# Optimization experiments

Measured on AMD Instinct MI355X. Metric: run time of the kernel, lower is better.

The kernel has to match this reference:

```python
import jax, jax.numpy as jnp
import numpy as np

B, S, H = 2, 2048, 2048
NH, NKV, D = 16, 4, 128      # heads, kv heads, head_dim
GROUPS = NH // NKV
WIN = 1024                    # sliding window
EPS = 1e-5
THETA = 10000.0
NEG = -1e9


def _rms_norm(x, w):
    # over last dim (head_dim)
    var = jnp.mean(x * x, axis=-1, keepdims=True)
    return x * jax.lax.rsqrt(var + EPS) * w


def _rotate_half(x):
    x1, x2 = jnp.split(x, 2, axis=-1)
    return jnp.concatenate([-x2, x1], axis=-1)


def _apply_rope(q, k, cos, sin):
    # q: [B,NH,S,D], k: [B,NKV,S,D], cos/sin: [B,S,D]
    c = cos[:, None, :, :]
    s = sin[:, None, :, :]
    q = q * c + _rotate_half(q) * s
    k = k * c + _rotate_half(k) * s
    return q, k


def setup_inputs() -> dict:
    key = jax.random.key(0)
    ks = jax.random.split(key, 8)
    std = 0.02
    hidden_states = jax.random.normal(ks[0], (B, S, H), dtype=jnp.float32)
    Wq = jax.random.normal(ks[1], (NH * D, H), dtype=jnp.float32) * std
    Wk = jax.random.normal(ks[2], (NKV * D, H), dtype=jnp.float32) * std
    Wv = jax.random.normal(ks[3], (NKV * D, H), dtype=jnp.float32) * std
    Wo = jax.random.normal(ks[4], (H, NH * D), dtype=jnp.float32) * std
    Wg = jax.random.normal(ks[5], (NH * D, H), dtype=jnp.float32) * std
    q_norm_w = jnp.ones((D,), dtype=jnp.float32)
    k_norm_w = jnp.ones((D,), dtype=jnp.float32)
    # RoPE tables
    inv_freq = 1.0 / (THETA ** (jnp.arange(0, D, 2, dtype=jnp.float32) / D))
    pos = jnp.arange(S, dtype=jnp.float32)
    freqs = jnp.einsum('s,d->sd', pos, inv_freq)          # [S, D/2]
    emb = jnp.concatenate([freqs, freqs], axis=-1)        # [S, D]
    cos = jnp.broadcast_to(jnp.cos(emb)[None], (B, S, D)).astype(jnp.float32)
    sin = jnp.broadcast_to(jnp.sin(emb)[None], (B, S, D)).astype(jnp.float32)
    i = jnp.arange(S)[:, None]
    j = jnp.arange(S)[None, :]
    allowed = (j <= i) & (i - j < WIN)
    attention_mask = jnp.where(allowed, 0.0, NEG).astype(jnp.float32)[None, None]  # [1,1,S,S]
    return {
        'hidden_states': hidden_states, 'cos': cos, 'sin': sin,
        'attention_mask': attention_mask,
        'Wq': Wq, 'Wk': Wk, 'Wv': Wv, 'Wo': Wo, 'Wg': Wg,
        'q_norm_w': q_norm_w, 'k_norm_w': k_norm_w,
    }


def reference(hidden_states, cos, sin, attention_mask, Wq, Wk, Wv, Wo, Wg, q_norm_w, k_norm_w):
    x = hidden_states                                  # [B,S,H]
    q = (x @ Wq.T).reshape(B, S, NH, D)
    k = (x @ Wk.T).reshape(B, S, NKV, D)
    v = (x @ Wv.T).reshape(B, S, NKV, D)
    gate = x @ Wg.T                                    # [B,S,NH*D]
    q = _rms_norm(q, q_norm_w)
    k = _rms_norm(k, k_norm_w)
    q = q.transpose(0, 2, 1, 3)                        # [B,NH,S,D]
    k = k.transpose(0, 2, 1, 3)                        # [B,NKV,S,D]
    v = v.transpose(0, 2, 1, 3)
    # local (sliding) attention layer -> RoPE applied
    q, k = _apply_rope(q, k, cos, sin)
    # GQA: repeat kv heads
    k = jnp.repeat(k, GROUPS, axis=1)                  # [B,NH,S,D]
    v = jnp.repeat(v, GROUPS, axis=1)
    scaling = D ** -0.5
    scores = jnp.einsum('bhqd,bhkd->bhqk', q, k) * scaling
    scores = scores + attention_mask                   # broadcast [1,1,S,S]
    probs = jax.nn.softmax(scores.astype(jnp.float32), axis=-1).astype(q.dtype)
    out = jnp.einsum('bhqk,bhkd->bhqd', probs, v)      # [B,NH,S,D]
    out = out.transpose(0, 2, 1, 3).reshape(B, S, NH * D)
    out = out * jax.nn.sigmoid(gate)
    return out @ Wo.T                                  # [B,S,H]
```

## Files before the change

### kernel.cpp

```cpp
#include <hip/hip_runtime.h>
#include <hip/hip_bf16.h>

#define B_    2
#define S_    2048
#define H_    2048
#define NH_   16
#define NKV_  4
#define D_    128
#define WIN_  1024

typedef __attribute__((ext_vector_type(8))) short short8;
typedef __attribute__((ext_vector_type(4))) float f32x4;

__device__ __forceinline__ void gl2lds16(const void* g, void* l) {
  __builtin_amdgcn_global_load_lds(
      (const __attribute__((address_space(1))) void*)g,
      (__attribute__((address_space(3))) void*)l, 16, 0, 0);
}

__device__ __forceinline__ unsigned short f2bf(float x) {
  union { float f; unsigned int u; } v; v.f = x;
  unsigned int r = v.u + 0x7fffu + ((v.u >> 16) & 1u);
  return (unsigned short)(r >> 16);
}
__device__ __forceinline__ float bf2f(unsigned short u) {
  union { unsigned int i; float f; } v; v.i = ((unsigned int)u) << 16; return v.f;
}

#define CVT_TOTAL 5767168L
__global__ __launch_bounds__(256) void convert_all(
    const float* __restrict__ hs, const float* __restrict__ wq,
    const float* __restrict__ wk, const float* __restrict__ wv,
    const float* __restrict__ wg, const float* __restrict__ wo,
    unsigned short* __restrict__ xb, unsigned short* __restrict__ wall,
    unsigned short* __restrict__ wob) {
  long i = (long)blockIdx.x * 256 + threadIdx.x;
  if (i >= CVT_TOTAL) return;
  const float4* src; ushort4* dst;
  if (i < 2097152)      { src = (const float4*)hs + i;                         dst = (ushort4*)xb + i; }
  else if (i < 3145728) { long j = i - 2097152; src = (const float4*)wq + j;   dst = (ushort4*)wall + j; }
  else if (i < 3407872) { long j = i - 3145728; src = (const float4*)wk + j;   dst = (ushort4*)wall + 1048576 + j; }
  else if (i < 3670016) { long j = i - 3407872; src = (const float4*)wv + j;   dst = (ushort4*)wall + 1310720 + j; }
  else if (i < 4718592) { long j = i - 3670016; src = (const float4*)wg + j;   dst = (ushort4*)wall + 1572864 + j; }
  else                  { long j = i - 4718592; src = (const float4*)wo + j;   dst = (ushort4*)wob + j; }
  float4 v = *src;
  ushort4 o; o.x = f2bf(v.x); o.y = f2bf(v.y); o.z = f2bf(v.z); o.w = f2bf(v.w);
  *dst = o;
}

template <bool OUT_BF16>
__global__ __launch_bounds__(256) void gemm_bt(
    const unsigned short* __restrict__ A,
    const unsigned short* __restrict__ Bm,
    void* __restrict__ Cv, int M, int N, int K)
{
  __shared__ unsigned short As[128 * 64];
  __shared__ unsigned short Bs[128 * 64];
  const int t = threadIdx.x;
  const int lane = t & 63, wave = t >> 6;
  const int quad = lane >> 4, rl = lane & 15;
  const int bm = blockIdx.x * 128, bn = blockIdx.y * 128;
  const int wm = (wave >> 1) * 64, wn = (wave & 1) * 64;
  const int ldsbase = (t & ~63) * 8;

  f32x4 acc[4][4];
#pragma unroll
  for (int i = 0; i < 4; i++)
#pragma unroll
    for (int j = 0; j < 4; j++) acc[i][j] = (f32x4){0.f, 0.f, 0.f, 0.f};

  for (int k0 = 0; k0 < K; k0 += 64) {
#pragma unroll
    for (int i = 0; i < 4; i++) {
      int tt = i * 256 + t;
      int row = tt >> 3;
      int lc = (tt & 7) ^ (row & 7);
      gl2lds16(A + (long)(bm + row) * K + k0 + lc * 8, As + i * 2048 + ldsbase);
      gl2lds16(Bm + (long)(bn + row) * K + k0 + lc * 8, Bs + i * 2048 + ldsbase);
    }
    __syncthreads();
#pragma unroll
    for (int kk = 0; kk < 2; kk++) {
      short8 af[4], bfr[4];
#pragma unroll
      for (int i = 0; i < 4; i++) {
        int row = wm + i * 16 + rl;
        af[i] = *(const short8*)(As + row * 64 + (((kk * 4 + quad) ^ (row & 7)) * 8));
      }
#pragma unroll
      for (int j = 0; j < 4; j++) {
        int row = wn + j * 16 + rl;
        bfr[j] = *(const short8*)(Bs + row * 64 + (((kk * 4 + quad) ^ (row & 7)) * 8));
      }
#pragma unroll
      for (int i = 0; i < 4; i++)
#pragma unroll
        for (int j = 0; j < 4; j++)
          acc[i][j] = __builtin_amdgcn_mfma_f32_16x16x32_bf16(af[i], bfr[j], acc[i][j], 0, 0, 0);
    }
    __syncthreads();
  }
#pragma unroll
  for (int i = 0; i < 4; i++) {
    int row0 = bm + wm + i * 16 + quad * 4;
#pragma unroll
    for (int j = 0; j < 4; j++) {
      int col = bn + wn + j * 16 + rl;
#pragma unroll
      for (int r = 0; r < 4; r++) {
        if (OUT_BF16)
          ((unsigned short*)Cv)[(long)(row0 + r) * N + col] = f2bf(acc[i][j][r]);
        else
          ((float*)Cv)[(long)(row0 + r) * N + col] = acc[i][j][r];
      }
    }
  }
}

__global__ __launch_bounds__(256) void pack_and_transpose(
    const unsigned short* __restrict__ qkvg,
    const float* __restrict__ cosb, const float* __restrict__ sinb,
    const float* __restrict__ qw, const float* __restrict__ kw,
    unsigned short* __restrict__ qb, unsigned short* __restrict__ kb,
    unsigned short* __restrict__ vt)
{
  __shared__ unsigned short tile[64][136];
  int t = threadIdx.x;
  if (blockIdx.x >= 20480) {
    int blk = blockIdx.x - 20480;
    int st = blk & 31, kv = (blk >> 5) & 3, b = blk >> 7;
    int s0 = st * 64;
#pragma unroll
    for (int i = 0; i < 4; i++) {
      int idx = i * 256 + t;
      int r = idx >> 4, c = (idx & 15) * 8;
      short8 v = *(const short8*)(qkvg + (long)(b * S_ + s0 + r) * 5120 + 2560 + kv * 128 + c);
      *(short8*)(&tile[r][c]) = v;
    }
    __syncthreads();
    long vo = (long)(b * NKV_ + kv) * 128;
#pragma unroll
    for (int i = 0; i < 8; i++) {
      int idx = i * 256 + t;
      int d = idx >> 4, sc = idx & 15;
      ushort4 o;
      o.x = tile[sc * 4 + 0][d]; o.y = tile[sc * 4 + 1][d];
      o.z = tile[sc * 4 + 2][d]; o.w = tile[sc * 4 + 3][d];
      *(ushort4*)(vt + (vo + d) * S_ + s0 + sc * 4) = o;
    }
    return;
  }
  int lane = t & 63, wave = t >> 6;
  long gw = (long)blockIdx.x * 4 + wave;
  int hu = (int)(gw % 20);
  long bs = gw / 20;
  int b = (int)(bs / S_);
  int s = (int)(bs % S_);
  const unsigned short* row = qkvg + bs * 5120;

  bool isq = hu < 16;
  const unsigned short* base = isq ? (row + hu * 128) : (row + 2048 + (hu - 16) * 128);
  float x1 = bf2f(base[lane]), x2 = bf2f(base[lane + 64]);
  float ss = x1 * x1 + x2 * x2;
#pragma unroll
  for (int m = 1; m < 64; m <<= 1) ss += __shfl_xor(ss, m, 64);
  float inv = rsqrtf(ss * (1.0f / 128.0f) + 1e-5f);
  const float* w = isq ? qw : kw;
  float n1 = x1 * inv * w[lane], n2 = x2 * inv * w[lane + 64];
  const float* cp = cosb + bs * 128;
  const float* sp = sinb + bs * 128;
  float o1 = n1 * cp[lane] - n2 * sp[lane];
  float o2 = n2 * cp[lane + 64] + n1 * sp[lane + 64];
  if (isq) {
    long o = ((long)(b * NH_ + hu) * S_ + s) * 128;
    qb[o + lane] = f2bf(o1); qb[o + lane + 64] = f2bf(o2);
  } else {
    long o = ((long)(b * NKV_ + (hu - 16)) * S_ + s) * 128;
    kb[o + lane] = f2bf(o1); kb[o + lane + 64] = f2bf(o2);
  }
}

#define KSTR 136
#define VSTR 72
#define PSTR 68
__global__ __launch_bounds__(256, 3) void attn_kernel(
    const unsigned short* __restrict__ qb,
    const unsigned short* __restrict__ kbuf,
    const unsigned short* __restrict__ vt,
    const unsigned short* __restrict__ qkvg,
    unsigned short* __restrict__ aout)
{
  __shared__ unsigned short Ks[64 * KSTR];
  __shared__ unsigned short Vs[128 * VSTR];
  __shared__ unsigned short Ps[4][16 * PSTR];
  int t = threadIdx.x, lane = t & 63, wave = t >> 6;
  int quad = lane >> 4, rl = lane & 15;
  int blk = blockIdx.x;
  int qt = 31 - (blk >> 5);
  int qu = blk & 3;
  int kv = (blk >> 2) & 3;
  int b  = (blk >> 4) & 1;
  int h = kv * 4 + wave;
  int q0 = qt * 64 + qu * 16;

  const unsigned short* qhead = qb + (((long)(b * NH_ + h)) * S_) * 128;
  short8 qf[4];
#pragma unroll
  for (int ks = 0; ks < 4; ks++)
    qf[ks] = *(const short8*)(qhead + (long)(q0 + rl) * 128 + ks * 32 + quad * 8);

  f32x4 oacc[8];
#pragma unroll
  for (int j = 0; j < 8; j++) oacc[j] = (f32x4){0.f, 0.f, 0.f, 0.f};
  float m_r[4], l_r[4];
#pragma unroll
  for (int r = 0; r < 4; r++) { m_r[r] = -1e9f; l_r[r] = 0.f; }

  const unsigned short* kbase_p = kbuf + ((long)(b * NKV_ + kv)) * S_ * 128;
  const unsigned short* vbase_p = vt + ((long)(b * NKV_ + kv)) * 128 * S_;
  int t_lo = qt - 16; if (t_lo < 0) t_lo = 0;

  int kr[4], kc[4], vr[4], vc[4];
#pragma unroll
  for (int i = 0; i < 4; i++) {
    int idx = i * 256 + t;
    kr[i] = idx >> 4; kc[i] = (idx & 15) * 8;
    vr[i] = idx >> 3; vc[i] = (idx & 7) * 8;
  }

  {
    int kb0 = t_lo * 64;
    short8 kv0[4], vv0[4];
#pragma unroll
    for (int i = 0; i < 4; i++) {
      kv0[i] = *(const short8*)(kbase_p + (long)(kb0 + kr[i]) * 128 + kc[i]);
      vv0[i] = *(const short8*)(vbase_p + (long)vr[i] * S_ + kb0 + vc[i]);
    }
#pragma unroll
    for (int i = 0; i < 4; i++) {
      *(short8*)(Ks + kr[i] * KSTR + kc[i]) = kv0[i];
      *(short8*)(Vs + vr[i] * VSTR + vc[i]) = vv0[i];
    }
  }
  __syncthreads();

  const float scale = 0.08838834764831845f;
  for (int kt = t_lo; kt <= qt; ++kt) {
    int kb0 = kt * 64;
    short8 kpre[4], vpre[4];
    if (kt < qt) {
      int nb0 = kb0 + 64;
#pragma unroll
      for (int i = 0; i < 4; i++) {
        kpre[i] = *(const short8*)(kbase_p + (long)(nb0 + kr[i]) * 128 + kc[i]);
        vpre[i] = *(const short8*)(vbase_p + (long)vr[i] * S_ + nb0 + vc[i]);
      }
    }

    f32x4 sc[4];
    __builtin_amdgcn_s_setprio(1);
#pragma unroll
    for (int nt = 0; nt < 4; nt++) {
      f32x4 c0 = (f32x4){0.f, 0.f, 0.f, 0.f};
#pragma unroll
      for (int ks = 0; ks < 4; ks++) {
        short8 bfrag = *(const short8*)(Ks + (nt * 16 + rl) * KSTR + (ks * 4 + quad) * 8);
        c0 = __builtin_amdgcn_mfma_f32_16x16x32_bf16(qf[ks], bfrag, c0, 0, 0, 0);
      }
      sc[nt] = c0;
    }
    __builtin_amdgcn_s_setprio(0);

#pragma unroll
    for (int nt = 0; nt < 4; nt++)
#pragma unroll
      for (int r = 0; r < 4; r++) {
        int i_row = q0 + quad * 4 + r;
        int j_col = kb0 + nt * 16 + rl;
        bool ok = (j_col <= i_row) && (i_row - j_col < WIN_);
        sc[nt][r] = ok ? sc[nt][r] * scale : -1e9f;
      }

    float mx[4];
#pragma unroll
    for (int r = 0; r < 4; r++) {
      float m0 = fmaxf(fmaxf(sc[0][r], sc[1][r]), fmaxf(sc[2][r], sc[3][r]));
#pragma unroll
      for (int m = 1; m < 16; m <<= 1) m0 = fmaxf(m0, __shfl_xor(m0, m, 64));
      mx[r] = m0;
    }
    bool need = (mx[0] > m_r[0]) | (mx[1] > m_r[1]) |
                (mx[2] > m_r[2]) | (mx[3] > m_r[3]);
    if (__any(need)) {
#pragma unroll
      for (int r = 0; r < 4; r++) {
        float newm = fmaxf(m_r[r], mx[r]);
        float alpha = __expf(m_r[r] - newm);
        l_r[r] *= alpha;
#pragma unroll
        for (int j = 0; j < 8; j++) oacc[j][r] *= alpha;
        m_r[r] = newm;
      }
    }
#pragma unroll
    for (int r = 0; r < 4; r++) {
      float p0 = __expf(sc[0][r] - m_r[r]), p1 = __expf(sc[1][r] - m_r[r]);
      float p2 = __expf(sc[2][r] - m_r[r]), p3 = __expf(sc[3][r] - m_r[r]);
      float rs = p0 + p1 + p2 + p3;
#pragma unroll
      for (int m = 1; m < 16; m <<= 1) rs += __shfl_xor(rs, m, 64);
      l_r[r] += rs;
      unsigned short* pw = &Ps[wave][(quad * 4 + r) * PSTR];
      pw[0 * 16 + rl] = f2bf(p0);
      pw[1 * 16 + rl] = f2bf(p1);
      pw[2 * 16 + rl] = f2bf(p2);
      pw[3 * 16 + rl] = f2bf(p3);
    }

    __builtin_amdgcn_s_setprio(1);
#pragma unroll
    for (int ks2 = 0; ks2 < 2; ks2++) {
      short8 af = *(const short8*)(&Ps[wave][rl * PSTR + (ks2 * 4 + quad) * 8]);
#pragma unroll
      for (int j = 0; j < 8; j++) {
        short8 bf2 = *(const short8*)(Vs + (j * 16 + rl) * VSTR + (ks2 * 4 + quad) * 8);
        oacc[j] = __builtin_amdgcn_mfma_f32_16x16x32_bf16(af, bf2, oacc[j], 0, 0, 0);
      }
    }
    __builtin_amdgcn_s_setprio(0);

    if (kt < qt) {
      __syncthreads();
#pragma unroll
      for (int i = 0; i < 4; i++) {
        *(short8*)(Ks + kr[i] * KSTR + kc[i]) = kpre[i];
        *(short8*)(Vs + vr[i] * VSTR + vc[i]) = vpre[i];
      }
      __syncthreads();
    }
  }

#pragma unroll
  for (int r = 0; r < 4; r++) {
    int s_idx = q0 + quad * 4 + r;
    float invl = 1.0f / l_r[r];
    long rowoff = (long)(b * S_ + s_idx);
    const unsigned short* gptr = qkvg + rowoff * 5120 + 3072 + h * 128;
    unsigned short* orow = aout + rowoff * 2048 + h * 128;
#pragma unroll
    for (int j = 0; j < 8; j++) {
      int d = j * 16 + rl;
      float o = oacc[j][r] * invl;
      float g = bf2f(gptr[d]);
      o = o / (1.0f + __expf(-g));
      orow[d] = f2bf(o);
    }
  }
}

extern "C" void kernel_launch(void* const* d_in, const int* in_sizes, int n_in,
                              void* d_out, int out_size, void* d_ws, size_t ws_size,
                              hipStream_t stream) {
  (void)in_sizes; (void)n_in; (void)out_size; (void)ws_size;
  const float* hs   = (const float*)d_in[0];
  const float* cosb = (const float*)d_in[1];
  const float* sinb = (const float*)d_in[2];
  const float* Wq = (const float*)d_in[4];
  const float* Wk = (const float*)d_in[5];
  const float* Wv = (const float*)d_in[6];
  const float* Wo = (const float*)d_in[7];
  const float* Wg = (const float*)d_in[8];
  const float* qw = (const float*)d_in[9];
  const float* kw = (const float*)d_in[10];
  float* out = (float*)d_out;

  char* ws = (char*)d_ws;
  unsigned short* Xb   = (unsigned short*)ws; ws += (size_t)4096 * 2048 * 2;
  unsigned short* Wall = (unsigned short*)ws; ws += (size_t)5120 * 2048 * 2;
  unsigned short* Wob  = (unsigned short*)ws; ws += (size_t)2048 * 2048 * 2;
  unsigned short* qkvg = (unsigned short*)ws; ws += (size_t)4096 * 5120 * 2;
  unsigned short* qb   = (unsigned short*)ws; ws += (size_t)B_ * NH_ * S_ * D_ * 2;
  unsigned short* kbuf = (unsigned short*)ws; ws += (size_t)B_ * NKV_ * S_ * D_ * 2;
  unsigned short* vtb  = (unsigned short*)ws; ws += (size_t)B_ * NKV_ * S_ * D_ * 2;
  unsigned short* aout = (unsigned short*)ws; ws += (size_t)4096 * 2048 * 2;

  convert_all<<<(int)((CVT_TOTAL + 255) / 256), 256, 0, stream>>>(
      hs, Wq, Wk, Wv, Wg, Wo, Xb, Wall, Wob);
  gemm_bt<true><<<dim3(32, 40), 256, 0, stream>>>(Xb, Wall, (void*)qkvg, 4096, 5120, 2048);
  pack_and_transpose<<<20736, 256, 0, stream>>>(qkvg, cosb, sinb, qw, kw, qb, kbuf, vtb);
  attn_kernel<<<1024, 256, 0, stream>>>(qb, kbuf, vtb, qkvg, aout);
  gemm_bt<false><<<dim3(32, 16), 256, 0, stream>>>(aout, Wob, (void*)out, 4096, 2048, 2048);
}
```

Before: 393.4 us.

## Add double-buffered 256x320-tile GEMM for fused QKV/gate projection

```diff
diff --git a/kernel.cpp b/kernel.cpp
--- a/kernel.cpp
+++ b/kernel.cpp
@@ -48,14 +48,115 @@
   *dst = o;
 }
 
+#define VMCNT0 asm volatile("s_waitcnt vmcnt(0)" ::: "memory")
+#define VMCNT2 asm volatile("s_waitcnt vmcnt(2)" ::: "memory")
+#define VMCNT3 asm volatile("s_waitcnt vmcnt(3)" ::: "memory")
+#define SBAR   asm volatile("s_barrier" ::: "memory")
+
+__global__ __launch_bounds__(512, 2) void gemm_qkvg(
+    const unsigned short* __restrict__ A,
+    const unsigned short* __restrict__ Bm,
+    unsigned short* __restrict__ C)
+{
+  const int KQ = 2048, NQ = 5120;
+  __shared__ unsigned short As[2][256 * 64];
+  __shared__ unsigned short Bs[2][320 * 64];
+  const int t = threadIdx.x;
+  const int lane = t & 63;
+  const int wave = t >> 6;
+  const int quad = lane >> 4, rl = lane & 15;
+  const int bm = blockIdx.x * 256, bn = blockIdx.y * 320;
+  const int wm = (wave >> 2) * 128, wn = (wave & 3) * 80;
+  const int wub = (t & ~63) * 8;
+
+#define STAGE_A_(d, k0, rd) { int cc = (rd) * 512 + t; int row = cc >> 3;      \
+    int lc = (cc & 7) ^ (row & 7);                                             \
+    gl2lds16(A + (long)(bm + row) * KQ + (k0) + lc * 8,                        \
+             &As[d][(rd) * 4096 + wub]); }
+#define STAGE_B_(d, k0, rd) { int cc = (rd) * 512 + t; int row = cc >> 3;      \
+    int lc = (cc & 7) ^ (row & 7);                                             \
+    gl2lds16(Bm + (long)(bn + row) * KQ + (k0) + lc * 8,                       \
+             &Bs[d][(rd) * 4096 + wub]); }
+#define RD_B(c, kk) { _Pragma("unroll") for (int j = 0; j < 5; j++) {          \
+    int row = wn + j * 16 + rl;                                                \
+    bfr[j] = *(const short8*)(&Bs[c][row * 64 + ((((kk)*4+quad)^(row&7))*8)]); } }
+#define RD_A(c, kk, f0) { _Pragma("unroll") for (int f = 0; f < 4; f++) {      \
+    int row = wm + ((f0) + f) * 16 + rl;                                       \
+    af[f] = *(const short8*)(&As[c][row * 64 + ((((kk)*4+quad)^(row&7))*8)]); } }
+#define MM(f0) { __builtin_amdgcn_s_setprio(1);                                \
+    _Pragma("unroll") for (int f = 0; f < 4; f++)                              \
+    _Pragma("unroll") for (int j = 0; j < 5; j++)                              \
+      acc[(f0)+f][j] = __builtin_amdgcn_mfma_f32_16x16x32_bf16(                \
+          af[f], bfr[j], acc[(f0)+f][j], 0, 0, 0);                             \
+    __builtin_amdgcn_s_setprio(0); }
+
+  f32x4 acc[8][5];
+#pragma unroll
+  for (int f = 0; f < 8; f++)
+#pragma unroll
+    for (int j = 0; j < 5; j++) acc[f][j] = (f32x4){0.f, 0.f, 0.f, 0.f};
+
+  STAGE_B_(0, 0, 0); STAGE_B_(0, 0, 1); STAGE_B_(0, 0, 2);
+  STAGE_B_(0, 0, 3); STAGE_B_(0, 0, 4);
+  STAGE_A_(0, 0, 0); STAGE_A_(0, 0, 2);
+  STAGE_A_(0, 0, 1); STAGE_A_(0, 0, 3);
+  VMCNT2; SBAR;
+
+  for (int tk = 0; tk < 32; ++tk) {
+    const int c = tk & 1, d = c ^ 1;
+    const int nk0 = tk * 64 + 64;
+    const bool hn = tk < 31;
+    short8 af[4], bfr[5];
+    RD_B(c, 0); RD_A(c, 0, 0);
+    if (hn) { STAGE_B_(d, nk0, 0); STAGE_B_(d, nk0, 1); STAGE_B_(d, nk0, 2); }
+    SBAR;
+    MM(0);
+    if (hn) { VMCNT3; } else { VMCNT0; }
+    SBAR;
+    RD_A(c, 0, 4);
+    if (hn) { STAGE_B_(d, nk0, 3); STAGE_B_(d, nk0, 4); }
+    SBAR;
+    MM(4);
+    SBAR;
+    RD_B(c, 1); RD_A(c, 1, 0);
+    if (hn) { STAGE_A_(d, nk0, 0); STAGE_A_(d, nk0, 2); }
+    SBAR;
+    MM(0);
+    SBAR;
+    RD_A(c, 1, 4);
+    if (hn) { STAGE_A_(d, nk0, 1); STAGE_A_(d, nk0, 3); }
+    SBAR;
+    MM(4);
+    if (hn) { VMCNT2; }
+    SBAR;
+  }
+
+#pragma unroll
+  for (int f = 0; f < 8; f++) {
+    int row0 = bm + wm + f * 16 + quad * 4;
+#pragma unroll
+    for (int j = 0; j < 5; j++) {
+      int col = bn + wn + j * 16 + rl;
+#pragma unroll
+      for (int r = 0; r < 4; r++)
+        C[(long)(row0 + r) * NQ + col] = f2bf(acc[f][j][r]);
+    }
+  }
+#undef STAGE_A_
+#undef STAGE_B_
+#undef RD_B
+#undef RD_A
+#undef MM
+}
+
 template <bool OUT_BF16>
 __global__ __launch_bounds__(256) void gemm_bt(
     const unsigned short* __restrict__ A,
     const unsigned short* __restrict__ Bm,
     void* __restrict__ Cv, int M, int N, int K)
 {
-  __shared__ unsigned short As[128 * 64];
-  __shared__ unsigned short Bs[128 * 64];
+  __shared__ unsigned short Asl[128 * 64];
+  __shared__ unsigned short Bsl[128 * 64];
   const int t = threadIdx.x;
   const int lane = t & 63, wave = t >> 6;
   const int quad = lane >> 4, rl = lane & 15;
@@ -75,8 +176,8 @@
       int tt = i * 256 + t;
       int row = tt >> 3;
       int lc = (tt & 7) ^ (row & 7);
-      gl2lds16(A + (long)(bm + row) * K + k0 + lc * 8, As + i * 2048 + ldsbase);
-      gl2lds16(Bm + (long)(bn + row) * K + k0 + lc * 8, Bs + i * 2048 + ldsbase);
+      gl2lds16(A + (long)(bm + row) * K + k0 + lc * 8, Asl + i * 2048 + ldsbase);
+      gl2lds16(Bm + (long)(bn + row) * K + k0 + lc * 8, Bsl + i * 2048 + ldsbase);
     }
     __syncthreads();
 #pragma unroll
@@ -85,12 +186,12 @@
 #pragma unroll
       for (int i = 0; i < 4; i++) {
         int row = wm + i * 16 + rl;
-        af[i] = *(const short8*)(As + row * 64 + (((kk * 4 + quad) ^ (row & 7)) * 8));
+        af[i] = *(const short8*)(Asl + row * 64 + (((kk * 4 + quad) ^ (row & 7)) * 8));
       }
 #pragma unroll
       for (int j = 0; j < 4; j++) {
         int row = wn + j * 16 + rl;
-        bfr[j] = *(const short8*)(Bs + row * 64 + (((kk * 4 + quad) ^ (row & 7)) * 8));
+        bfr[j] = *(const short8*)(Bsl + row * 64 + (((kk * 4 + quad) ^ (row & 7)) * 8));
       }
 #pragma unroll
       for (int i = 0; i < 4; i++)
@@ -386,7 +487,7 @@
 
   convert_all<<<(int)((CVT_TOTAL + 255) / 256), 256, 0, stream>>>(
       hs, Wq, Wk, Wv, Wg, Wo, Xb, Wall, Wob);
-  gemm_bt<true><<<dim3(32, 40), 256, 0, stream>>>(Xb, Wall, (void*)qkvg, 4096, 5120, 2048);
+  gemm_qkvg<<<dim3(16, 16), 512, 0, stream>>>(Xb, Wall, qkvg);
   pack_and_transpose<<<20736, 256, 0, stream>>>(qkvg, cosb, sinb, qw, kw, qb, kbuf, vtb);
   attn_kernel<<<1024, 256, 0, stream>>>(qb, kbuf, vtb, qkvg, aout);
   gemm_bt<false><<<dim3(32, 16), 256, 0, stream>>>(aout, Wob, (void*)out, 4096, 2048, 2048);
```

Result: faster. 369.3 us (-6.1%).
